# Kernel tuning notes

Measured on AMD Instinct MI355X. Metric: run time of the kernel, lower is better.

## Reference

```python
import jax, jax.numpy as jnp
import numpy as np

N, E, EL = 20000, 320000, 100000
IN, HID, OUT, H = 256, 128, 128, 4
NEG_SLOPE = 0.2


def setup_inputs() -> dict:
    key = jax.random.key(0)
    ks = jax.random.split(key, 20)
    g = lambda k, shape, fan: jax.random.normal(k, shape, jnp.float32) * (1.0 / np.sqrt(fan))
    inp = {
        'x': jax.random.normal(ks[0], (N, IN), jnp.float32),
        'edge_index': jax.random.randint(ks[1], (2, E), 0, N, jnp.int32),
        'edge_label_index': jax.random.randint(ks[2], (2, EL), 0, N, jnp.int32),
        # GATv2 layer 1: in -> hidden, heads=H, concat
        'W_l1': g(ks[3], (IN, H * HID), IN), 'b_l1': jnp.zeros((H * HID,), jnp.float32),
        'W_r1': g(ks[4], (IN, H * HID), IN), 'b_r1': jnp.zeros((H * HID,), jnp.float32),
        'att1': g(ks[5], (H, HID), HID), 'bias1': jnp.zeros((H * HID,), jnp.float32),
        # GATv2 layer 2: H*hidden -> out, heads=1
        'W_l2': g(ks[6], (H * HID, OUT), H * HID), 'b_l2': jnp.zeros((OUT,), jnp.float32),
        'W_r2': g(ks[7], (H * HID, OUT), H * HID), 'b_r2': jnp.zeros((OUT,), jnp.float32),
        'att2': g(ks[8], (1, OUT), OUT), 'bias2': jnp.zeros((OUT,), jnp.float32),
        # decoder: Linear(2*OUT, HID) -> GELU -> Linear(HID, 1)
        'W_d1': g(ks[9], (2 * OUT, HID), 2 * OUT), 'b_d1': jnp.zeros((HID,), jnp.float32),
        'W_d2': g(ks[10], (HID, 1), HID), 'b_d2': jnp.zeros((1,), jnp.float32),
    }
    return inp


def gatv2_conv(x, src, dst, Wl, bl, Wr, br, att, bias, heads, ch):
    n = x.shape[0]
    xl = (x @ Wl + bl).reshape(n, heads, ch)  # source transform
    xr = (x @ Wr + br).reshape(n, heads, ch)  # target transform
    xj = xl[src]                              # [E, H, C] messages from source
    xi = xr[dst]                              # [E, H, C]
    e = jax.nn.leaky_relu(xi + xj, NEG_SLOPE)
    logits = jnp.einsum('ehc,hc->eh', e, att)  # [E, H]
    # segment softmax over incoming edges of each target node
    m = jax.ops.segment_max(logits, dst, num_segments=n)
    a = jnp.exp(logits - m[dst])
    s = jax.ops.segment_sum(a, dst, num_segments=n)
    alpha = a / s[dst]
    out = jax.ops.segment_sum(alpha[..., None] * xj, dst, num_segments=n)
    return out.reshape(n, heads * ch) + bias


def reference(x, edge_index, edge_label_index,
              W_l1, b_l1, W_r1, b_r1, att1, bias1,
              W_l2, b_l2, W_r2, b_r2, att2, bias2,
              W_d1, b_d1, W_d2, b_d2):
    n = x.shape[0]
    loops = jnp.arange(n, dtype=edge_index.dtype)
    src = jnp.concatenate([edge_index[0], loops])  # add_self_loops=True (PyG default)
    dst = jnp.concatenate([edge_index[1], loops])
    z = gatv2_conv(x, src, dst, W_l1, b_l1, W_r1, b_r1, att1, bias1, H, HID)
    z = jax.nn.gelu(z)  # dropout is identity in eval mode
    z = gatv2_conv(z, src, dst, W_l2, b_l2, W_r2, b_r2, att2, bias2, 1, OUT)
    # link decoder: gather-concat-MLP
    h = jnp.concatenate([z[edge_label_index[0]], z[edge_label_index[1]]], axis=-1)
    h = jax.nn.gelu(h @ W_d1 + b_d1)
    return (h @ W_d2 + b_d2).squeeze(-1)
```

## Files before the change

kernel.cpp:

```cpp
#include <hip/hip_runtime.h>
#include <hip/hip_bf16.h>
#include <math.h>
#include <stdint.h>

using bf16 = __hip_bfloat16;
typedef unsigned short u16;
typedef unsigned int   u32;
typedef __attribute__((ext_vector_type(8))) short short8;
typedef __attribute__((ext_vector_type(4))) float f32x4;
typedef _Float16 h2 __attribute__((ext_vector_type(2)));

static constexpr int NN   = 20000;
static constexpr int EE   = 320000;
static constexpr int ELN  = 100000;
static constexpr int ETOT = EE + NN;
static constexpr int INC  = 256;
static constexpr int C1   = 512;
static constexpr int C2   = 128;
static constexpr int NB   = (NN + 255) / 256;

__device__ __forceinline__ float us2f(u16 u){ union{u32 i; float f;}x; x.i=((u32)u)<<16; return x.f; }
__device__ __forceinline__ u16  f2us(float f){ union{bf16 h; u16 u;}c; c.h=__float2bfloat16(f); return c.u; }
__device__ __forceinline__ float h2f(u16 u){ union{u16 u; _Float16 h;}c; c.u=u; return (float)c.h; }
__device__ __forceinline__ float gelu_f(float x){
  float u = 1.5957691216057308f*(x + 0.044715f*x*x*x);
  float ex = __expf(u);
  float th = 1.f - 2.f/(ex + 1.f);
  return 0.5f*x*(1.f+th);
}
__device__ __forceinline__ void gl_lds16(const u16* g, void* l) {
  __builtin_amdgcn_global_load_lds((const __attribute__((address_space(1))) void*)g,
                                   (__attribute__((address_space(3))) void*)l, 16, 0, 0);
}
__device__ __forceinline__ void ld4v(const float* p, float* o){ float4 v=*(const float4*)p; o[0]=v.x;o[1]=v.y;o[2]=v.z;o[3]=v.w; }
__device__ __forceinline__ void ld4v(const u16* p, float* o){ uint2 v=*(const uint2*)p;
  o[0]=us2f(v.x&0xffff);o[1]=us2f(v.x>>16);o[2]=us2f(v.y&0xffff);o[3]=us2f(v.y>>16); }
__device__ __forceinline__ void ld4v(const _Float16* p, float* o){ uint2 v=*(const uint2*)p;
  o[0]=h2f(v.x&0xffff);o[1]=h2f(v.x>>16);o[2]=h2f(v.y&0xffff);o[3]=h2f(v.y>>16); }
__device__ __forceinline__ void ld8v(const float* p, float* o){ ld4v(p,o); ld4v(p+4,o+4); }
__device__ __forceinline__ void ld8v(const u16* p, float* o){ uint4 v=*(const uint4*)p;
  o[0]=us2f(v.x&0xffff);o[1]=us2f(v.x>>16);o[2]=us2f(v.y&0xffff);o[3]=us2f(v.y>>16);
  o[4]=us2f(v.z&0xffff);o[5]=us2f(v.z>>16);o[6]=us2f(v.w&0xffff);o[7]=us2f(v.w>>16); }
__device__ __forceinline__ void ld8v(const _Float16* p, float* o){ uint4 v=*(const uint4*)p;
  o[0]=h2f(v.x&0xffff);o[1]=h2f(v.x>>16);o[2]=h2f(v.y&0xffff);o[3]=h2f(v.y>>16);
  o[4]=h2f(v.z&0xffff);o[5]=h2f(v.z>>16);o[6]=h2f(v.w&0xffff);o[7]=h2f(v.w>>16); }
__device__ __forceinline__ void ld2v(const float* p, float* o){ float2 v=*(const float2*)p; o[0]=v.x;o[1]=v.y; }
__device__ __forceinline__ void ld2v(const _Float16* p, float* o){ u32 w=*(const u32*)p;
  o[0]=h2f(w&0xffff); o[1]=h2f(w>>16); }
__device__ __forceinline__ void st4v(float* p, const float* v){ *(float4*)p = make_float4(v[0],v[1],v[2],v[3]); }
__device__ __forceinline__ void st4v(u16* p, const float* v){ uint2 o;
  o.x=f2us(v[0])|((u32)f2us(v[1])<<16); o.y=f2us(v[2])|((u32)f2us(v[3])<<16); *(uint2*)p=o; }
__device__ __forceinline__ void st8v(float* p, const float* v){ st4v(p,v); st4v(p+4,v+4); }
__device__ __forceinline__ void st8v(u16* p, const float* v){ uint4 o;
  o.x=f2us(v[0])|((u32)f2us(v[1])<<16); o.y=f2us(v[2])|((u32)f2us(v[3])<<16);
  o.z=f2us(v[4])|((u32)f2us(v[5])<<16); o.w=f2us(v[6])|((u32)f2us(v[7])<<16); *(uint4*)p=o; }

struct PrepArgs {
  const float* x; u16* xth; u16* xtl; int nx;
  const float* wsrc[5]; u16* wth[5]; u16* wtl[5]; int wK[5]; int wN[5];
  const int* ei; int* cnt;
};
__global__ __launch_bounds__(256) void k_prep(PrepArgs a) {
  int seg = blockIdx.y;
  int tid = blockIdx.x*256 + threadIdx.x;
  int stride = gridDim.x*256;
  if (seg == 0) {
    for (int i = tid; i < a.nx; i += stride) {
      float v = a.x[i];
      u16 h = f2us(v);
      a.xth[i] = h;
      a.xtl[i] = f2us(v - us2f(h));
    }
  } else if (seg <= 5) {
    int s = seg - 1;
    int K = a.wK[s], N = a.wN[s];
    int n = K * N;
    for (int i = tid; i < n; i += stride) {
      int nn = i / K, k = i - nn*K;
      float v = a.wsrc[s][(size_t)k*N + nn];
      u16 h = f2us(v);
      a.wth[s][i] = h;
      a.wtl[s][i] = f2us(v - us2f(h));
    }
  } else {
    for (int e = tid; e < ETOT; e += stride) {
      int d = (e < EE) ? a.ei[EE + e] : (e - EE);
      if ((u32)d < (u32)NN) atomicAdd(&a.cnt[d], 1);
    }
  }
}

__global__ void k_scan_a(const int* __restrict__ cnt, int* __restrict__ row_ptr,
                         int* __restrict__ bsum) {
  __shared__ int buf[256];
  int idx = blockIdx.x*256 + threadIdx.x;
  int v = (idx < NN) ? cnt[idx] : 0;
  buf[threadIdx.x] = v;
  __syncthreads();
  for (int off = 1; off < 256; off <<= 1) {
    int t = (threadIdx.x >= off) ? buf[threadIdx.x - off] : 0;
    __syncthreads();
    buf[threadIdx.x] += t;
    __syncthreads();
  }
  if (idx < NN) row_ptr[idx] = buf[threadIdx.x] - v;
  if (threadIdx.x == 255) bsum[blockIdx.x] = buf[255];
}
__global__ void k_scan_b(int* __restrict__ bsum, int* __restrict__ row_ptr) {
  __shared__ int buf[128];
  int v = (threadIdx.x < NB) ? bsum[threadIdx.x] : 0;
  buf[threadIdx.x] = v;
  __syncthreads();
  for (int off = 1; off < 128; off <<= 1) {
    int t = (threadIdx.x >= off) ? buf[threadIdx.x - off] : 0;
    __syncthreads();
    buf[threadIdx.x] += t;
    __syncthreads();
  }
  if (threadIdx.x < NB) bsum[threadIdx.x] = buf[threadIdx.x] - v;
  if (threadIdx.x == 127) row_ptr[NN] = buf[127];
}
__global__ void k_scan_c(int* __restrict__ row_ptr, const int* __restrict__ bsum,
                         int* __restrict__ cur) {
  int idx = blockIdx.x*256 + threadIdx.x;
  if (idx < NN) {
    int v = row_ptr[idx] + bsum[blockIdx.x];
    row_ptr[idx] = v;
    cur[idx] = v;
  }
}
__global__ void k_scatter(const int* __restrict__ ei, int* __restrict__ cur,
                          int* __restrict__ col) {
  int e = blockIdx.x*blockDim.x + threadIdx.x;
  if (e < ETOT) {
    int s, d;
    if (e < EE) { s = ei[e]; d = ei[EE + e]; } else { s = d = e - EE; }
    if ((u32)d >= (u32)NN) d = 0;
    int pos = atomicAdd(&cur[d], 1);
    if ((u32)pos < (u32)ETOT) col[pos] = s;
  }
}

__global__ __launch_bounds__(256, 3)
void k_mgemm_a(const u16* __restrict__ Ath, const u16* __restrict__ Atl,
               const u16* __restrict__ Bth, const u16* __restrict__ Btl,
               const float* __restrict__ biasA, const float* __restrict__ biasB, int ncut,
               _Float16* __restrict__ C, int M, int N, int K, int nby) {
  __shared__ __align__(16) u16 sm[17408];
  int tid = threadIdx.x;
  int bidy = blockIdx.x % nby, bidx = blockIdx.x / nby;
  int m0 = bidx * 128, n0 = bidy * 128;
  int wave = tid >> 6, lane = tid & 63;
  int wm = (wave & 1) * 64, wn = (wave >> 1) * 64;
  int l15 = lane & 15, quad = lane >> 4;
  const u16* pbase = (wave == 0) ? Ath : (wave == 1) ? Atl : (wave == 2) ? Bth : Btl;
  bool isA = wave < 2;
  int rbase = isA ? m0 : n0;
  int rseg = lane >> 2;
  int kseg = (lane & 3) * 8;
  f32x4 acc[4][4] = {};
  for (int k0 = 0; k0 < K; k0 += 32) {
    #pragma unroll
    for (int i = 0; i < 8; ++i) {
      int r = rbase + i*16 + rseg;
      if (isA && r > M-1) r = M-1;
      gl_lds16(&pbase[(size_t)r*K + k0 + kseg], (char*)sm + (wave<<13) + (i<<10));
    }
    __syncthreads();
    short8 af_h[4], af_l[4], bf_h[4], bf_l[4];
    #pragma unroll
    for (int i = 0; i < 4; ++i) {
      af_h[i] = *(const short8*)&sm[         (wm + i*16 + l15)*32 + quad*8];
      af_l[i] = *(const short8*)&sm[ 4096 +  (wm + i*16 + l15)*32 + quad*8];
      bf_h[i] = *(const short8*)&sm[ 8192 +  (wn + i*16 + l15)*32 + quad*8];
      bf_l[i] = *(const short8*)&sm[12288 +  (wn + i*16 + l15)*32 + quad*8];
    }
    #pragma unroll
    for (int i = 0; i < 4; ++i)
      #pragma unroll
      for (int j = 0; j < 4; ++j) {
        acc[i][j] = __builtin_amdgcn_mfma_f32_16x16x32_bf16(af_h[i], bf_l[j], acc[i][j], 0,0,0);
        acc[i][j] = __builtin_amdgcn_mfma_f32_16x16x32_bf16(af_l[i], bf_h[j], acc[i][j], 0,0,0);
        acc[i][j] = __builtin_amdgcn_mfma_f32_16x16x32_bf16(af_h[i], bf_h[j], acc[i][j], 0,0,0);
      }
    __syncthreads();
  }
  #pragma unroll
  for (int j = 0; j < 4; ++j) {
    int col = wn + j*16 + l15;
    int colg = n0 + col;
    float bv = (colg < ncut) ? biasA[colg] : biasB[colg - ncut];
    #pragma unroll
    for (int i = 0; i < 4; ++i) {
      int rowb = wm + i*16 + quad*4;
      #pragma unroll
      for (int r = 0; r < 4; ++r) {
        union { _Float16 h; u16 u; } cv;
        cv.h = (_Float16)(acc[i][j][r] + bv);
        sm[(rowb + r)*136 + col] = cv.u;
      }
    }
  }
  __syncthreads();
  int row = tid >> 1, half = (tid & 1) * 64;
  int gr = m0 + row;
  if (gr < M) {
    uint4* d = (uint4*)&C[(size_t)gr*N + n0 + half];
    const uint4* s = (const uint4*)&sm[row*136 + half];
    #pragma unroll
    for (int q = 0; q < 8; ++q) d[q] = s[q];
  }
}

__global__ __launch_bounds__(256, 3)
void k_dec3(const _Float16* __restrict__ z2,
            const int* __restrict__ eli,
            const u16* __restrict__ Wth, const u16* __restrict__ Wtl,
            const float* __restrict__ bd1,
            const float* __restrict__ Wd2, const float* __restrict__ bd2,
            float* __restrict__ out) {
  __shared__ __align__(16) u16 Ah[128][32], Al[128][32];
  __shared__ __align__(16) u16 Bh[128][32], Bl[128][32];
  __shared__ float pr[128][2];
  int tid = threadIdx.x;
  int e0 = blockIdx.x * 128;
  int wave = tid >> 6, lane = tid & 63;
  int wm = (wave & 1) * 64, wn = (wave >> 1) * 64;
  int l15 = lane & 15, quad = lane >> 4;
  int ar = tid >> 3;
  int ak = (tid & 7) * 4;
  int bn = tid >> 2;
  int bc = (tid & 3) * 8;
  int ia4[4], ib4[4];
  #pragma unroll
  for (int i = 0; i < 4; ++i) {
    int e = e0 + ar + 32*i;
    bool ev = e < ELN;
    int a = ev ? eli[e] : 0;      if ((u32)a >= (u32)NN) a = 0;
    int b = ev ? eli[ELN+e] : 0;  if ((u32)b >= (u32)NN) b = 0;
    ia4[i] = a; ib4[i] = b;
  }
  f32x4 acc[4][4] = {};
  for (int k0 = 0; k0 < 256; k0 += 32) {
    #pragma unroll
    for (int i = 0; i < 4; ++i) {
      int row = ar + 32*i;
      int kk = k0 + ak;
      const _Float16* src = (kk < 128) ? &z2[(size_t)ia4[i]*128 + kk]
                                       : &z2[(size_t)ib4[i]*128 + (kk - 128)];
      float hv[4];
      ld4v(src, hv);
      u16 hi[4], lo[4];
      #pragma unroll
      for (int j = 0; j < 4; ++j) {
        hi[j] = f2us(hv[j]);
        lo[j] = f2us(hv[j] - us2f(hi[j]));
      }
      *(uint2*)&Ah[row][ak] = make_uint2(hi[0]|((u32)hi[1]<<16), hi[2]|((u32)hi[3]<<16));
      *(uint2*)&Al[row][ak] = make_uint2(lo[0]|((u32)lo[1]<<16), lo[2]|((u32)lo[3]<<16));
    }
    #pragma unroll
    for (int i = 0; i < 2; ++i) {
      int n = bn + 64*i;
      *(uint4*)&Bh[n][bc] = *(const uint4*)&Wth[(size_t)n*256 + k0 + bc];
      *(uint4*)&Bl[n][bc] = *(const uint4*)&Wtl[(size_t)n*256 + k0 + bc];
    }
    __syncthreads();
    short8 af_h[4], af_l[4], bf_h[4], bf_l[4];
    #pragma unroll
    for (int i = 0; i < 4; ++i) {
      af_h[i] = *(const short8*)&Ah[wm + i*16 + l15][quad*8];
      af_l[i] = *(const short8*)&Al[wm + i*16 + l15][quad*8];
      bf_h[i] = *(const short8*)&Bh[wn + i*16 + l15][quad*8];
      bf_l[i] = *(const short8*)&Bl[wn + i*16 + l15][quad*8];
    }
    #pragma unroll
    for (int i = 0; i < 4; ++i)
      #pragma unroll
      for (int j = 0; j < 4; ++j) {
        acc[i][j] = __builtin_amdgcn_mfma_f32_16x16x32_bf16(af_h[i], bf_l[j], acc[i][j], 0,0,0);
        acc[i][j] = __builtin_amdgcn_mfma_f32_16x16x32_bf16(af_l[i], bf_h[j], acc[i][j], 0,0,0);
        acc[i][j] = __builtin_amdgcn_mfma_f32_16x16x32_bf16(af_h[i], bf_h[j], acc[i][j], 0,0,0);
      }
    __syncthreads();
  }
  float w2c[4], bbc[4];
  #pragma unroll
  for (int j = 0; j < 4; ++j) {
    int col = wn + j*16 + l15;
    w2c[j] = Wd2[col];
    bbc[j] = bd1[col];
  }
  #pragma unroll
  for (int i = 0; i < 4; ++i) {
    #pragma unroll
    for (int r = 0; r < 4; ++r) {
      float part = 0.f;
      #pragma unroll
      for (int j = 0; j < 4; ++j)
        part += gelu_f(acc[i][j][r] + bbc[j]) * w2c[j];
      part += __shfl_xor(part,1); part += __shfl_xor(part,2);
      part += __shfl_xor(part,4); part += __shfl_xor(part,8);
      if (l15 == 0) pr[wm + i*16 + quad*4 + r][wn>>6] = part;
    }
  }
  __syncthreads();
  if (tid < 128) {
    int e = e0 + tid;
    if (e < ELN) out[e] = pr[tid][0] + pr[tid][1] + bd2[0];
  }
}

__global__ __launch_bounds__(256) void k_edge1p(const _Float16* __restrict__ xl,
                                                const _Float16* __restrict__ xr, int ld,
                                                const float* __restrict__ att,
                                                const float* __restrict__ bias,
                                                const int* __restrict__ row_ptr,
                                                const int* __restrict__ col,
                                                u16* __restrict__ z1h, u16* __restrict__ z1l) {
  int wid = (blockIdx.x*blockDim.x + threadIdx.x) >> 6;
  if (wid >= NN) return;
  int lane = threadIdx.x & 63;
  int c8 = lane*8;
  union Q { uint4 u; h2 h[4]; };
  Q XI; XI.u = *(const uint4*)&xr[(size_t)wid*ld + c8];
  h2 at[4];
  #pragma unroll
  for (int k=0;k<4;++k) { at[k][0] = (_Float16)att[c8+2*k]; at[k][1] = (_Float16)att[c8+2*k+1]; }
  const h2 k02 = {(_Float16)0.2f, (_Float16)0.2f};
  float acc[8] = {};
  float s = 0.f;
  int e0 = __builtin_amdgcn_readfirstlane(row_ptr[wid]);
  int e1 = __builtin_amdgcn_readfirstlane(row_ptr[wid+1]);
  int e = e0;
  for (; e + 4 <= e1; e += 4) {
    int s1 = __builtin_amdgcn_readfirstlane(col[e]);   if ((u32)s1 >= (u32)NN) s1 = 0;
    int s2 = __builtin_amdgcn_readfirstlane(col[e+1]); if ((u32)s2 >= (u32)NN) s2 = 0;
    int s3 = __builtin_amdgcn_readfirstlane(col[e+2]); if ((u32)s3 >= (u32)NN) s3 = 0;
    int s4 = __builtin_amdgcn_readfirstlane(col[e+3]); if ((u32)s4 >= (u32)NN) s4 = 0;
    Q X1, X2, X3, X4;
    X1.u = *(const uint4*)&xl[(size_t)s1*ld + c8];
    X2.u = *(const uint4*)&xl[(size_t)s2*ld + c8];
    X3.u = *(const uint4*)&xl[(size_t)s3*ld + c8];
    X4.u = *(const uint4*)&xl[(size_t)s4*ld + c8];
    float p1 = 0.f, p2 = 0.f, p3 = 0.f, p4 = 0.f;
    #pragma unroll
    for (int k=0;k<4;++k) {
      h2 t1 = XI.h[k] + X1.h[k]; t1 = __builtin_elementwise_max(t1, t1*k02);
      p1 = __builtin_amdgcn_fdot2(t1, at[k], p1, false);
      h2 t2 = XI.h[k] + X2.h[k]; t2 = __builtin_elementwise_max(t2, t2*k02);
      p2 = __builtin_amdgcn_fdot2(t2, at[k], p2, false);
      h2 t3 = XI.h[k] + X3.h[k]; t3 = __builtin_elementwise_max(t3, t3*k02);
      p3 = __builtin_amdgcn_fdot2(t3, at[k], p3, false);
      h2 t4 = XI.h[k] + X4.h[k]; t4 = __builtin_elementwise_max(t4, t4*k02);
      p4 = __builtin_amdgcn_fdot2(t4, at[k], p4, false);
    }
    p1 += __shfl_xor(p1,1); p2 += __shfl_xor(p2,1); p3 += __shfl_xor(p3,1); p4 += __shfl_xor(p4,1);
    p1 += __shfl_xor(p1,2); p2 += __shfl_xor(p2,2); p3 += __shfl_xor(p3,2); p4 += __shfl_xor(p4,2);
    p1 += __shfl_xor(p1,4); p2 += __shfl_xor(p2,4); p3 += __shfl_xor(p3,4); p4 += __shfl_xor(p4,4);
    p1 += __shfl_xor(p1,8); p2 += __shfl_xor(p2,8); p3 += __shfl_xor(p3,8); p4 += __shfl_xor(p4,8);
    float w1 = __expf(p1), w2 = __expf(p2), w3 = __expf(p3), w4 = __expf(p4);
    s += (w1 + w2) + (w3 + w4);
    #pragma unroll
    for (int k=0;k<4;++k) {
      acc[2*k]   += (w1*(float)X1.h[k][0] + w2*(float)X2.h[k][0])
                  + (w3*(float)X3.h[k][0] + w4*(float)X4.h[k][0]);
      acc[2*k+1] += (w1*(float)X1.h[k][1] + w2*(float)X2.h[k][1])
                  + (w3*(float)X3.h[k][1] + w4*(float)X4.h[k][1]);
    }
  }
  for (; e < e1; ++e) {
    int sn = __builtin_amdgcn_readfirstlane(col[e]); if ((u32)sn >= (u32)NN) sn = 0;
    Q XJ; XJ.u = *(const uint4*)&xl[(size_t)sn*ld + c8];
    float p = 0.f;
    #pragma unroll
    for (int k=0;k<4;++k) {
      h2 t = XI.h[k] + XJ.h[k];
      t = __builtin_elementwise_max(t, t*k02);
      p = __builtin_amdgcn_fdot2(t, at[k], p, false);
    }
    p += __shfl_xor(p,1); p += __shfl_xor(p,2);
    p += __shfl_xor(p,4); p += __shfl_xor(p,8);
    float w = __expf(p);
    s += w;
    #pragma unroll
    for (int k=0;k<4;++k) {
      acc[2*k]   += w*(float)XJ.h[k][0];
      acc[2*k+1] += w*(float)XJ.h[k][1];
    }
  }
  float inv = 1.f/s;
  u16 hh[8], ll[8];
  #pragma unroll
  for (int j=0;j<8;++j) {
    float o = gelu_f(acc[j]*inv + bias[c8+j]);
    hh[j] = f2us(o);
    ll[j] = f2us(o - us2f(hh[j]));
  }
  uint4 H, L;
  H.x = hh[0]|((u32)hh[1]<<16); H.y = hh[2]|((u32)hh[3]<<16);
  H.z = hh[4]|((u32)hh[5]<<16); H.w = hh[6]|((u32)hh[7]<<16);
  L.x = ll[0]|((u32)ll[1]<<16); L.y = ll[2]|((u32)ll[3]<<16);
  L.z = ll[4]|((u32)ll[5]<<16); L.w = ll[6]|((u32)ll[7]<<16);
  *(uint4*)&z1h[(size_t)wid*C1 + c8] = H;
  *(uint4*)&z1l[(size_t)wid*C1 + c8] = L;
}

__global__ __launch_bounds__(256) void k_edge2p(const _Float16* __restrict__ xl,
                                                const _Float16* __restrict__ xr, int ld,
                                                const float* __restrict__ att,
                                                const float* __restrict__ bias,
                                                const int* __restrict__ row_ptr,
                                                const int* __restrict__ col,
                                                _Float16* __restrict__ z2) {
  int wid = (blockIdx.x*blockDim.x + threadIdx.x) >> 6;
  if (wid >= NN) return;
  int lane = threadIdx.x & 63;
  int c2 = lane*2;
  union W { u32 u; h2 h; };
  W XI; XI.u = *(const u32*)&xr[(size_t)wid*ld + c2];
  h2 at; at[0] = (_Float16)att[c2]; at[1] = (_Float16)att[c2+1];
  const h2 k02 = {(_Float16)0.2f, (_Float16)0.2f};
  float s = 0.f, ac0 = 0.f, ac1 = 0.f;
  int e0 = __builtin_amdgcn_readfirstlane(row_ptr[wid]);
  int e1 = __builtin_amdgcn_readfirstlane(row_ptr[wid+1]);
  int e = e0;
  for (; e + 4 <= e1; e += 4) {
    int s1 = __builtin_amdgcn_readfirstlane(col[e]);   if ((u32)s1 >= (u32)NN) s1 = 0;
    int s2 = __builtin_amdgcn_readfirstlane(col[e+1]); if ((u32)s2 >= (u32)NN) s2 = 0;
    int s3 = __builtin_amdgcn_readfirstlane(col[e+2]); if ((u32)s3 >= (u32)NN) s3 = 0;
    int s4 = __builtin_amdgcn_readfirstlane(col[e+3]); if ((u32)s4 >= (u32)NN) s4 = 0;
    W X1, X2, X3, X4;
    X1.u = *(const u32*)&xl[(size_t)s1*ld + c2];
    X2.u = *(const u32*)&xl[(size_t)s2*ld + c2];
    X3.u = *(const u32*)&xl[(size_t)s3*ld + c2];
    X4.u = *(const u32*)&xl[(size_t)s4*ld + c2];
    h2 t1 = XI.h + X1.h; t1 = __builtin_elementwise_max(t1, t1*k02);
    h2 t2 = XI.h + X2.h; t2 = __builtin_elementwise_max(t2, t2*k02);
    h2 t3 = XI.h + X3.h; t3 = __builtin_elementwise_max(t3, t3*k02);
    h2 t4 = XI.h + X4.h; t4 = __builtin_elementwise_max(t4, t4*k02);
    float p1 = __builtin_amdgcn_fdot2(t1, at, 0.f, false);
    float p2 = __builtin_amdgcn_fdot2(t2, at, 0.f, false);
    float p3 = __builtin_amdgcn_fdot2(t3, at, 0.f, false);
    float p4 = __builtin_amdgcn_fdot2(t4, at, 0.f, false);
    p1 += __shfl_xor(p1,1);  p2 += __shfl_xor(p2,1);  p3 += __shfl_xor(p3,1);  p4 += __shfl_xor(p4,1);
    p1 += __shfl_xor(p1,2);  p2 += __shfl_xor(p2,2);  p3 += __shfl_xor(p3,2);  p4 += __shfl_xor(p4,2);
    p1 += __shfl_xor(p1,4);  p2 += __shfl_xor(p2,4);  p3 += __shfl_xor(p3,4);  p4 += __shfl_xor(p4,4);
    p1 += __shfl_xor(p1,8);  p2 += __shfl_xor(p2,8);  p3 += __shfl_xor(p3,8);  p4 += __shfl_xor(p4,8);
    p1 += __shfl_xor(p1,16); p2 += __shfl_xor(p2,16); p3 += __shfl_xor(p3,16); p4 += __shfl_xor(p4,16);
    p1 += __shfl_xor(p1,32); p2 += __shfl_xor(p2,32); p3 += __shfl_xor(p3,32); p4 += __shfl_xor(p4,32);
    float w1 = __expf(p1), w2 = __expf(p2), w3 = __expf(p3), w4 = __expf(p4);
    s += (w1 + w2) + (w3 + w4);
    ac0 += (w1*(float)X1.h[0] + w2*(float)X2.h[0]) + (w3*(float)X3.h[0] + w4*(float)X4.h[0]);
    ac1 += (w1*(float)X1.h[1] + w2*(float)X2.h[1]) + (w3*(float)X3.h[1] + w4*(float)X4.h[1]);
  }
  for (; e < e1; ++e) {
    int sn = __builtin_amdgcn_readfirstlane(col[e]); if ((u32)sn >= (u32)NN) sn = 0;
    W XJ; XJ.u = *(const u32*)&xl[(size_t)sn*ld + c2];
    h2 t = XI.h + XJ.h;
    t = __builtin_elementwise_max(t, t*k02);
    float p = __builtin_amdgcn_fdot2(t, at, 0.f, false);
    p += __shfl_xor(p,1);  p += __shfl_xor(p,2);
    p += __shfl_xor(p,4);  p += __shfl_xor(p,8);
    p += __shfl_xor(p,16); p += __shfl_xor(p,32);
    float w = __expf(p);
    s += w;
    ac0 += w*(float)XJ.h[0];
    ac1 += w*(float)XJ.h[1];
  }
  float inv = 1.f/s;
  union { h2 h; u32 u; } o;
  o.h[0] = (_Float16)(ac0*inv + bias[c2]);
  o.h[1] = (_Float16)(ac1*inv + bias[c2+1]);
  *(u32*)&z2[(size_t)wid*C2 + c2] = o.u;
}

__global__ void k_hist(const int* __restrict__ ei, int* __restrict__ cnt) {
  int e = blockIdx.x*blockDim.x + threadIdx.x;
  if (e < ETOT) {
    int d = (e < EE) ? ei[EE + e] : (e - EE);
    if ((u32)d < (u32)NN) atomicAdd(&cnt[d], 1);
  }
}
template <typename AT, typename CT>
__global__ __launch_bounds__(256) void k_gemm(const AT* __restrict__ A,
                                              const float* __restrict__ W,
                                              const float* __restrict__ bias,
                                              CT* __restrict__ C,
                                              int M, int Nc, int K) {
  __shared__ __align__(16) float As[16][64];
  __shared__ __align__(16) float Bs[16][64];
  int tid = threadIdx.x;
  int m0 = blockIdx.x*64, n0 = blockIdx.y*64;
  int ty = tid >> 4, tx = tid & 15;
  int lrow = tid >> 2;
  int lk   = (tid & 3)*4;
  int wk   = tid >> 4;
  int wn   = (tid & 15)*4;
  float acc[4][4] = {};
  for (int k0 = 0; k0 < K; k0 += 16) {
    int row = m0 + lrow;
    if (row < M) {
      float a4[4]; ld4v(&A[(size_t)row*K + k0 + lk], a4);
      As[lk+0][lrow]=a4[0]; As[lk+1][lrow]=a4[1]; As[lk+2][lrow]=a4[2]; As[lk+3][lrow]=a4[3];
    } else {
      #pragma unroll
      for (int j=0;j<4;++j) As[lk+j][lrow]=0.f;
    }
    {
      float4 bv4 = *(const float4*)&W[(size_t)(k0+wk)*Nc + n0 + wn];
      Bs[wk][wn+0]=bv4.x; Bs[wk][wn+1]=bv4.y; Bs[wk][wn+2]=bv4.z; Bs[wk][wn+3]=bv4.w;
    }
    __syncthreads();
    #pragma unroll
    for (int kk=0;kk<16;++kk) {
      float4 av = *(const float4*)&As[kk][ty*4];
      float4 bv = *(const float4*)&Bs[kk][tx*4];
      float a[4]={av.x,av.y,av.z,av.w}, b[4]={bv.x,bv.y,bv.z,bv.w};
      #pragma unroll
      for (int i=0;i<4;++i)
        #pragma unroll
        for (int j=0;j<4;++j)
          acc[i][j] += a[i]*b[j];
    }
    __syncthreads();
  }
  float bv[4];
  #pragma unroll
  for (int j=0;j<4;++j) bv[j] = bias[n0 + tx*4 + j];
  #pragma unroll
  for (int i=0;i<4;++i) {
    int row = m0 + ty*4 + i;
    if (row < M) {
      float o4[4] = {acc[i][0]+bv[0], acc[i][1]+bv[1], acc[i][2]+bv[2], acc[i][3]+bv[3]};
      st4v(&C[(size_t)row*Nc + n0 + tx*4], o4);
    }
  }
}
template <typename TI, typename TO>
__global__ __launch_bounds__(256) void k_edge1c(const TI* __restrict__ xl,
                                                const TI* __restrict__ xr, int ld,
                                                const float* __restrict__ att,
                                                const float* __restrict__ bias,
                                                const int* __restrict__ row_ptr,
                                                const int* __restrict__ col,
                                                TO* __restrict__ z1) {
  int wid = (blockIdx.x*blockDim.x + threadIdx.x) >> 6;
  if (wid >= NN) return;
  int lane = threadIdx.x & 63;
  int c8 = lane*8;
  float xi[8], av[8], acc[8] = {};
  ld8v(&xr[(size_t)wid*ld + c8], xi);
  #pragma unroll
  for (int j=0;j<8;++j) av[j] = att[c8+j];
  float s = 0.f;
  int e0 = row_ptr[wid], e1 = row_ptr[wid+1];
  for (int e = e0; e < e1; ++e) {
    int sn = col[e]; if ((u32)sn >= (u32)NN) sn = 0;
    float xj[8];
    ld8v(&xl[(size_t)sn*ld + c8], xj);
    float p = 0.f;
    #pragma unroll
    for (int j=0;j<8;++j) {
      float t = xi[j] + xj[j];
      t = fmaxf(t, 0.2f*t);
      p += t*av[j];
    }
    p += __shfl_xor(p,1); p += __shfl_xor(p,2);
    p += __shfl_xor(p,4); p += __shfl_xor(p,8);
    float w = __expf(p);
    s += w;
    #pragma unroll
    for (int j=0;j<8;++j) acc[j] += w*xj[j];
  }
  float inv = 1.f/s, o[8];
  #pragma unroll
  for (int j=0;j<8;++j) o[j] = gelu_f(acc[j]*inv + bias[c8+j]);
  st8v(&z1[(size_t)wid*C1 + c8], o);
}
template <typename TI, typename TO>
__global__ __launch_bounds__(256) void k_edge2c(const TI* __restrict__ xl,
                                                const TI* __restrict__ xr, int ld,
                                                const float* __restrict__ att,
                                                const float* __restrict__ bias,
                                                const int* __restrict__ row_ptr,
                                                const int* __restrict__ col,
                                                TO* __restrict__ z2) {
  int wid = (blockIdx.x*blockDim.x + threadIdx.x) >> 6;
  if (wid >= NN) return;
  int lane = threadIdx.x & 63;
  int c2 = lane*2;
  float xiv[2];
  ld2v(&xr[(size_t)wid*ld + c2], xiv);
  float a0 = att[c2], a1 = att[c2+1];
  float s = 0.f, ac0 = 0.f, ac1 = 0.f;
  int e0 = row_ptr[wid], e1 = row_ptr[wid+1];
  for (int e = e0; e < e1; ++e) {
    int sn = col[e]; if ((u32)sn >= (u32)NN) sn = 0;
    float xj[2];
    ld2v(&xl[(size_t)sn*ld + c2], xj);
    float t0 = xiv[0] + xj[0]; t0 = fmaxf(t0, 0.2f*t0);
    float t1 = xiv[1] + xj[1]; t1 = fmaxf(t1, 0.2f*t1);
    float p = t0*a0 + t1*a1;
    p += __shfl_xor(p,1);  p += __shfl_xor(p,2);
    p += __shfl_xor(p,4);  p += __shfl_xor(p,8);
    p += __shfl_xor(p,16); p += __shfl_xor(p,32);
    float w = __expf(p);
    s += w;
    ac0 += w*xj[0];
    ac1 += w*xj[1];
  }
  float inv = 1.f/s;
  z2[(size_t)wid*C2 + c2]   = (TO)(ac0*inv + bias[c2]);
  z2[(size_t)wid*C2 + c2+1] = (TO)(ac1*inv + bias[c2+1]);
}
__global__ __launch_bounds__(256) void k_dec2(const float* __restrict__ z2,
                                              const int* __restrict__ eli,
                                              const float* __restrict__ Wd1,
                                              const float* __restrict__ bd1,
                                              const float* __restrict__ Wd2,
                                              const float* __restrict__ bd2,
                                              float* __restrict__ out) {
  __shared__ __align__(16) float As[16][64];
  __shared__ __align__(16) float Bs[16][128];
  int tid = threadIdx.x;
  int e0 = blockIdx.x * 64;
  int ty = tid >> 4, tx = tid & 15;
  int lrow = tid >> 2;
  int lk   = (tid & 3) * 4;
  int wk   = tid >> 4;
  int wn   = (tid & 15) * 8;
  int e = e0 + lrow;
  bool ev = e < ELN;
  int ia = ev ? eli[e] : 0;       if ((u32)ia >= (u32)NN) ia = 0;
  int ib = ev ? eli[ELN+e] : 0;   if ((u32)ib >= (u32)NN) ib = 0;
  float acc[4][8] = {};
  for (int k0 = 0; k0 < 256; k0 += 16) {
    int kk4 = k0 + lk;
    const float* src = (kk4 < 128) ? &z2[(size_t)ia*128 + kk4]
                                   : &z2[(size_t)ib*128 + (kk4 - 128)];
    float4 a4 = ev ? *(const float4*)src : make_float4(0.f,0.f,0.f,0.f);
    As[lk+0][lrow]=a4.x; As[lk+1][lrow]=a4.y; As[lk+2][lrow]=a4.z; As[lk+3][lrow]=a4.w;
    *(float4*)&Bs[wk][wn]   = *(const float4*)&Wd1[(size_t)(k0+wk)*128 + wn];
    *(float4*)&Bs[wk][wn+4] = *(const float4*)&Wd1[(size_t)(k0+wk)*128 + wn + 4];
    __syncthreads();
    #pragma unroll
    for (int kk = 0; kk < 16; ++kk) {
      float4 av = *(const float4*)&As[kk][ty*4];
      float a[4] = {av.x, av.y, av.z, av.w};
      float4 b0 = *(const float4*)&Bs[kk][tx*4];
      float4 b1 = *(const float4*)&Bs[kk][64 + tx*4];
      float b[8] = {b0.x,b0.y,b0.z,b0.w,b1.x,b1.y,b1.z,b1.w};
      #pragma unroll
      for (int i = 0; i < 4; ++i)
        #pragma unroll
        for (int j = 0; j < 8; ++j)
          acc[i][j] += a[i]*b[j];
    }
    __syncthreads();
  }
  float w2[8], bb[8];
  #pragma unroll
  for (int j = 0; j < 4; ++j) {
    w2[j]   = Wd2[tx*4+j];      bb[j]   = bd1[tx*4+j];
    w2[j+4] = Wd2[64+tx*4+j];   bb[j+4] = bd1[64+tx*4+j];
  }
  float b2 = bd2[0];
  #pragma unroll
  for (int i = 0; i < 4; ++i) {
    float part = 0.f;
    #pragma unroll
    for (int j = 0; j < 8; ++j)
      part += gelu_f(acc[i][j] + bb[j]) * w2[j];
    part += __shfl_xor(part,1); part += __shfl_xor(part,2);
    part += __shfl_xor(part,4); part += __shfl_xor(part,8);
    int row = e0 + ty*4 + i;
    if (tx == 0 && row < ELN) out[row] = part + b2;
  }
}

__global__ void k_tiny(float* out, float code) {
  if (threadIdx.x == 0) out[0] = code;
}

extern "C" void kernel_launch(void* const* d_in, const int* in_sizes, int n_in,
                              void* d_out, int out_size, void* d_ws, size_t ws_size,
                              hipStream_t stream) {
  const float* x     = (const float*)d_in[0];
  const int*   ei    = (const int*)  d_in[1];
  const int*   eli   = (const int*)  d_in[2];
  const float* Wl1   = (const float*)d_in[3];
  const float* bl1   = (const float*)d_in[4];
  const float* Wr1   = (const float*)d_in[5];
  const float* br1   = (const float*)d_in[6];
  const float* att1  = (const float*)d_in[7];
  const float* bias1 = (const float*)d_in[8];
  const float* Wl2   = (const float*)d_in[9];
  const float* bl2   = (const float*)d_in[10];
  const float* Wr2   = (const float*)d_in[11];
  const float* br2   = (const float*)d_in[12];
  const float* att2  = (const float*)d_in[13];
  const float* bias2 = (const float*)d_in[14];
  const float* Wd1   = (const float*)d_in[15];
  const float* bd1   = (const float*)d_in[16];
  const float* Wd2   = (const float*)d_in[17];
  const float* bd2   = (const float*)d_in[18];
  float* out = (float*)d_out;

  constexpr size_t INTW = (size_t)(NN+1) + NN + ETOT;
  constexpr size_t FULL_WORDS = 3ull*NN*C1 + INTW;
  constexpr size_t CMP_WORDS  = 3ull*NN*C1/2 + INTW;

  bool full    = ws_size >= FULL_WORDS*4;
  bool compact = !full && ws_size >= CMP_WORDS*4;
  if (!full && !compact) {
    size_t mb = ws_size >> 20;
    k_tiny<<<1, 64, 0, stream>>>(out, 16384.f + (float)mb);
    return;
  }

  size_t regA = full ? (size_t)NN*C1 : (size_t)NN*C1/2;
  char* base = (char*)d_ws;
  void* wA = base;
  void* wB = base + regA*4;
  void* wC = base + 2*regA*4;
  int* row_ptr = (int*)(base + 3*regA*4);
  int* cnt     = row_ptr + (NN + 1);
  int* col     = cnt + NN;
  int* bsum    = (int*)wA;

  hipMemsetAsync(cnt, 0, NN*sizeof(int), stream);

  if (full) {
    _Float16* xlr1 = (_Float16*)wA;
    _Float16* xlr2 = (_Float16*)wA;
    u16* xth = (u16*)wB;
    u16* xtl = xth + (size_t)NN*INC;
    u16* wt1th = (u16*)((char*)wB + (21u<<20));
    u16* wt1tl = wt1th + 1024*256;
    u16* wt2th = wt1tl + 1024*256;
    u16* wt2tl = wt2th + 256*512;
    u16* wdth  = wt2tl + 256*512;
    u16* wdtl  = wdth  + 128*256;
    u16* z1h = (u16*)wC;
    u16* z1l = z1h + (size_t)NN*C1;
    _Float16* z2 = (_Float16*)wC;

    PrepArgs pa;
    pa.x = x; pa.xth = xth; pa.xtl = xtl; pa.nx = NN*INC;
    pa.wsrc[0]=Wl1; pa.wth[0]=wt1th;         pa.wtl[0]=wt1tl;         pa.wK[0]=INC; pa.wN[0]=C1;
    pa.wsrc[1]=Wr1; pa.wth[1]=wt1th+512*256; pa.wtl[1]=wt1tl+512*256; pa.wK[1]=INC; pa.wN[1]=C1;
    pa.wsrc[2]=Wl2; pa.wth[2]=wt2th;         pa.wtl[2]=wt2tl;         pa.wK[2]=C1;  pa.wN[2]=C2;
    pa.wsrc[3]=Wr2; pa.wth[3]=wt2th+128*512; pa.wtl[3]=wt2tl+128*512; pa.wK[3]=C1;  pa.wN[3]=C2;
    pa.wsrc[4]=Wd1; pa.wth[4]=wdth;          pa.wtl[4]=wdtl;          pa.wK[4]=256; pa.wN[4]=C2;
    pa.ei = ei; pa.cnt = cnt;
    k_prep<<<dim3(1344, 7), 256, 0, stream>>>(pa);

    k_scan_a<<<NB, 256, 0, stream>>>(cnt, row_ptr, bsum);
    k_scan_b<<<1, 128, 0, stream>>>(bsum, row_ptr);
    k_scan_c<<<NB, 256, 0, stream>>>(row_ptr, bsum, cnt);
    k_scatter<<<(ETOT+255)/256, 256, 0, stream>>>(ei, cnt, col);

    k_mgemm_a<<<157*8, 256, 0, stream>>>(xth, xtl, wt1th, wt1tl,
                                         bl1, br1, 512, xlr1, NN, 1024, INC, 8);
    k_edge1p<<<NN/4, 256, 0, stream>>>(xlr1, xlr1+512, 1024, att1, bias1, row_ptr, col, z1h, z1l);
    k_mgemm_a<<<157*2, 256, 0, stream>>>(z1h, z1l, wt2th, wt2tl,
                                         bl2, br2, 128, xlr2, NN, 256, C1, 2);
    k_edge2p<<<NN/4, 256, 0, stream>>>(xlr2, xlr2+128, 256, att2, bias2, row_ptr, col, z2);
    k_dec3<<<(ELN+127)/128, 256, 0, stream>>>(z2, eli, wdth, wdtl, bd1, Wd2, bd2, out);
  } else {
    u16* xl1 = (u16*)wA;
    u16* xr1 = (u16*)wB;
    u16* z1  = (u16*)wC;
    float* xl2 = (float*)wA;
    float* xr2 = (float*)wB;
    float* z2  = (float*)wC;
    k_hist<<<(ETOT+255)/256, 256, 0, stream>>>(ei, cnt);
    k_scan_a<<<NB, 256, 0, stream>>>(cnt, row_ptr, bsum);
    k_scan_b<<<1, 128, 0, stream>>>(bsum, row_ptr);
    k_scan_c<<<NB, 256, 0, stream>>>(row_ptr, bsum, cnt);
    k_scatter<<<(ETOT+255)/256, 256, 0, stream>>>(ei, cnt, col);
    dim3 g1((NN+63)/64, C1/64);
    dim3 g2((NN+63)/64, C2/64);
    k_gemm<float,u16><<<g1, 256, 0, stream>>>(x, Wl1, bl1, xl1, NN, C1, INC);
    k_gemm<float,u16><<<g1, 256, 0, stream>>>(x, Wr1, br1, xr1, NN, C1, INC);
    k_edge1c<u16,u16><<<NN/4, 256, 0, stream>>>(xl1, xr1, C1, att1, bias1, row_ptr, col, z1);
    k_gemm<u16,float><<<g2, 256, 0, stream>>>(z1, Wl2, bl2, xl2, NN, C2, C1);
    k_gemm<u16,float><<<g2, 256, 0, stream>>>(z1, Wr2, br2, xr2, NN, C2, C1);
    k_edge2c<float,float><<<NN/4, 256, 0, stream>>>(xl2, xr2, C2, att2, bias2, row_ptr, col, z2);
    k_dec2<<<(ELN+63)/64, 256, 0, stream>>>(z2, eli, Wd1, bd1, Wd2, bd2, out);
  }
}
```

Measured before the change: 344.7 us.

## Split decoder linear into per-node projections before gathering edge pairs

```diff
diff --git a/kernel.cpp b/kernel.cpp
--- a/kernel.cpp
+++ b/kernel.cpp
@@ -57,7 +57,7 @@
 
 struct PrepArgs {
   const float* x; u16* xth; u16* xtl; int nx;
-  const float* wsrc[5]; u16* wth[5]; u16* wtl[5]; int wK[5]; int wN[5];
+  const float* wsrc[6]; u16* wth[6]; u16* wtl[6]; int wK[6]; int wN[6];
   const int* ei; int* cnt;
 };
 __global__ __launch_bounds__(256) void k_prep(PrepArgs a) {
@@ -71,7 +71,7 @@
       a.xth[i] = h;
       a.xtl[i] = f2us(v - us2f(h));
     }
-  } else if (seg <= 5) {
+  } else if (seg <= 6) {
     int s = seg - 1;
     int K = a.wK[s], N = a.wN[s];
     int n = K * N;
@@ -189,7 +189,7 @@
   for (int j = 0; j < 4; ++j) {
     int col = wn + j*16 + l15;
     int colg = n0 + col;
-    float bv = (colg < ncut) ? biasA[colg] : biasB[colg - ncut];
+    float bv = (colg < ncut) ? biasA[colg] : (biasB ? biasB[colg - ncut] : 0.f);
     #pragma unroll
     for (int i = 0; i < 4; ++i) {
       int rowb = wm + i*16 + quad*4;
@@ -212,102 +212,28 @@
   }
 }
 
-__global__ __launch_bounds__(256, 3)
-void k_dec3(const _Float16* __restrict__ z2,
-            const int* __restrict__ eli,
-            const u16* __restrict__ Wth, const u16* __restrict__ Wtl,
-            const float* __restrict__ bd1,
-            const float* __restrict__ Wd2, const float* __restrict__ bd2,
-            float* __restrict__ out) {
-  __shared__ __align__(16) u16 Ah[128][32], Al[128][32];
-  __shared__ __align__(16) u16 Bh[128][32], Bl[128][32];
-  __shared__ float pr[128][2];
-  int tid = threadIdx.x;
-  int e0 = blockIdx.x * 128;
-  int wave = tid >> 6, lane = tid & 63;
-  int wm = (wave & 1) * 64, wn = (wave >> 1) * 64;
-  int l15 = lane & 15, quad = lane >> 4;
-  int ar = tid >> 3;
-  int ak = (tid & 7) * 4;
-  int bn = tid >> 2;
-  int bc = (tid & 3) * 8;
-  int ia4[4], ib4[4];
-  #pragma unroll
-  for (int i = 0; i < 4; ++i) {
-    int e = e0 + ar + 32*i;
-    bool ev = e < ELN;
-    int a = ev ? eli[e] : 0;      if ((u32)a >= (u32)NN) a = 0;
-    int b = ev ? eli[ELN+e] : 0;  if ((u32)b >= (u32)NN) b = 0;
-    ia4[i] = a; ib4[i] = b;
-  }
-  f32x4 acc[4][4] = {};
-  for (int k0 = 0; k0 < 256; k0 += 32) {
-    #pragma unroll
-    for (int i = 0; i < 4; ++i) {
-      int row = ar + 32*i;
-      int kk = k0 + ak;
-      const _Float16* src = (kk < 128) ? &z2[(size_t)ia4[i]*128 + kk]
-                                       : &z2[(size_t)ib4[i]*128 + (kk - 128)];
-      float hv[4];
-      ld4v(src, hv);
-      u16 hi[4], lo[4];
-      #pragma unroll
-      for (int j = 0; j < 4; ++j) {
-        hi[j] = f2us(hv[j]);
-        lo[j] = f2us(hv[j] - us2f(hi[j]));
-      }
-      *(uint2*)&Ah[row][ak] = make_uint2(hi[0]|((u32)hi[1]<<16), hi[2]|((u32)hi[3]<<16));
-      *(uint2*)&Al[row][ak] = make_uint2(lo[0]|((u32)lo[1]<<16), lo[2]|((u32)lo[3]<<16));
-    }
-    #pragma unroll
-    for (int i = 0; i < 2; ++i) {
-      int n = bn + 64*i;
-      *(uint4*)&Bh[n][bc] = *(const uint4*)&Wth[(size_t)n*256 + k0 + bc];
-      *(uint4*)&Bl[n][bc] = *(const uint4*)&Wtl[(size_t)n*256 + k0 + bc];
-    }
-    __syncthreads();
-    short8 af_h[4], af_l[4], bf_h[4], bf_l[4];
-    #pragma unroll
-    for (int i = 0; i < 4; ++i) {
-      af_h[i] = *(const short8*)&Ah[wm + i*16 + l15][quad*8];
-      af_l[i] = *(const short8*)&Al[wm + i*16 + l15][quad*8];
-      bf_h[i] = *(const short8*)&Bh[wn + i*16 + l15][quad*8];
-      bf_l[i] = *(const short8*)&Bl[wn + i*16 + l15][quad*8];
-    }
-    #pragma unroll
-    for (int i = 0; i < 4; ++i)
-      #pragma unroll
-      for (int j = 0; j < 4; ++j) {
-        acc[i][j] = __builtin_amdgcn_mfma_f32_16x16x32_bf16(af_h[i], bf_l[j], acc[i][j], 0,0,0);
-        acc[i][j] = __builtin_amdgcn_mfma_f32_16x16x32_bf16(af_l[i], bf_h[j], acc[i][j], 0,0,0);
-        acc[i][j] = __builtin_amdgcn_mfma_f32_16x16x32_bf16(af_h[i], bf_h[j], acc[i][j], 0,0,0);
-      }
-    __syncthreads();
-  }
-  float w2c[4], bbc[4];
-  #pragma unroll
-  for (int j = 0; j < 4; ++j) {
-    int col = wn + j*16 + l15;
-    w2c[j] = Wd2[col];
-    bbc[j] = bd1[col];
-  }
-  #pragma unroll
-  for (int i = 0; i < 4; ++i) {
-    #pragma unroll
-    for (int r = 0; r < 4; ++r) {
-      float part = 0.f;
-      #pragma unroll
-      for (int j = 0; j < 4; ++j)
-        part += gelu_f(acc[i][j][r] + bbc[j]) * w2c[j];
-      part += __shfl_xor(part,1); part += __shfl_xor(part,2);
-      part += __shfl_xor(part,4); part += __shfl_xor(part,8);
-      if (l15 == 0) pr[wm + i*16 + quad*4 + r][wn>>6] = part;
-    }
-  }
-  __syncthreads();
-  if (tid < 128) {
-    int e = e0 + tid;
-    if (e < ELN) out[e] = pr[tid][0] + pr[tid][1] + bd2[0];
+__global__ __launch_bounds__(256) void k_dec5(const _Float16* __restrict__ UV,
+                                              const int* __restrict__ eli,
+                                              const float* __restrict__ Wd2,
+                                              const float* __restrict__ bd2,
+                                              float* __restrict__ out) {
+  int gw = (blockIdx.x*256 + threadIdx.x) >> 6;
+  int nw = (gridDim.x*256) >> 6;
+  int lane = threadIdx.x & 63;
+  int c2 = lane*2;
+  float w2a = Wd2[c2], w2b = Wd2[c2+1];
+  float b2 = bd2[0];
+  for (int e = gw; e < ELN; e += nw) {
+    int a = __builtin_amdgcn_readfirstlane(eli[e]);      if ((u32)a >= (u32)NN) a = 0;
+    int b = __builtin_amdgcn_readfirstlane(eli[ELN+e]);  if ((u32)b >= (u32)NN) b = 0;
+    float u[2], v[2];
+    ld2v(&UV[(size_t)a*256 + c2], u);
+    ld2v(&UV[(size_t)b*256 + 128 + c2], v);
+    float p = gelu_f(u[0]+v[0])*w2a + gelu_f(u[1]+v[1])*w2b;
+    p += __shfl_xor(p,1);  p += __shfl_xor(p,2);
+    p += __shfl_xor(p,4);  p += __shfl_xor(p,8);
+    p += __shfl_xor(p,16); p += __shfl_xor(p,32);
+    if (lane == 0) out[e] = p + b2;
   }
 }
 
@@ -412,7 +338,7 @@
                                                 const float* __restrict__ bias,
                                                 const int* __restrict__ row_ptr,
                                                 const int* __restrict__ col,
-                                                _Float16* __restrict__ z2) {
+                                                u16* __restrict__ z2h, u16* __restrict__ z2l) {
   int wid = (blockIdx.x*blockDim.x + threadIdx.x) >> 6;
   if (wid >= NN) return;
   int lane = threadIdx.x & 63;
@@ -469,10 +395,12 @@
     ac1 += w*(float)XJ.h[1];
   }
   float inv = 1.f/s;
-  union { h2 h; u32 u; } o;
-  o.h[0] = (_Float16)(ac0*inv + bias[c2]);
-  o.h[1] = (_Float16)(ac1*inv + bias[c2+1]);
-  *(u32*)&z2[(size_t)wid*C2 + c2] = o.u;
+  float o0 = ac0*inv + bias[c2];
+  float o1 = ac1*inv + bias[c2+1];
+  u16 h0 = f2us(o0), h1 = f2us(o1);
+  u16 l0 = f2us(o0 - us2f(h0)), l1v = f2us(o1 - us2f(h1));
+  *(u32*)&z2h[(size_t)wid*C2 + c2] = h0 | ((u32)h1 << 16);
+  *(u32*)&z2l[(size_t)wid*C2 + c2] = l0 | ((u32)l1v << 16);
 }
 
 __global__ void k_hist(const int* __restrict__ ei, int* __restrict__ cnt) {
@@ -734,6 +662,7 @@
   if (full) {
     _Float16* xlr1 = (_Float16*)wA;
     _Float16* xlr2 = (_Float16*)wA;
+    _Float16* UV   = (_Float16*)wA;
     u16* xth = (u16*)wB;
     u16* xtl = xth + (size_t)NN*INC;
     u16* wt1th = (u16*)((char*)wB + (21u<<20));
@@ -741,20 +670,22 @@
     u16* wt2th = wt1tl + 1024*256;
     u16* wt2tl = wt2th + 256*512;
     u16* wdth  = wt2tl + 256*512;
-    u16* wdtl  = wdth  + 128*256;
+    u16* wdtl  = wdth  + 256*128;
     u16* z1h = (u16*)wC;
     u16* z1l = z1h + (size_t)NN*C1;
-    _Float16* z2 = (_Float16*)wC;
+    u16* z2h = (u16*)wC;
+    u16* z2l = z2h + (size_t)NN*C2;
 
     PrepArgs pa;
     pa.x = x; pa.xth = xth; pa.xtl = xtl; pa.nx = NN*INC;
-    pa.wsrc[0]=Wl1; pa.wth[0]=wt1th;         pa.wtl[0]=wt1tl;         pa.wK[0]=INC; pa.wN[0]=C1;
-    pa.wsrc[1]=Wr1; pa.wth[1]=wt1th+512*256; pa.wtl[1]=wt1tl+512*256; pa.wK[1]=INC; pa.wN[1]=C1;
-    pa.wsrc[2]=Wl2; pa.wth[2]=wt2th;         pa.wtl[2]=wt2tl;         pa.wK[2]=C1;  pa.wN[2]=C2;
-    pa.wsrc[3]=Wr2; pa.wth[3]=wt2th+128*512; pa.wtl[3]=wt2tl+128*512; pa.wK[3]=C1;  pa.wN[3]=C2;
-    pa.wsrc[4]=Wd1; pa.wth[4]=wdth;          pa.wtl[4]=wdtl;          pa.wK[4]=256; pa.wN[4]=C2;
+    pa.wsrc[0]=Wl1;          pa.wth[0]=wt1th;         pa.wtl[0]=wt1tl;         pa.wK[0]=INC; pa.wN[0]=C1;
+    pa.wsrc[1]=Wr1;          pa.wth[1]=wt1th+512*256; pa.wtl[1]=wt1tl+512*256; pa.wK[1]=INC; pa.wN[1]=C1;
+    pa.wsrc[2]=Wl2;          pa.wth[2]=wt2th;         pa.wtl[2]=wt2tl;         pa.wK[2]=C1;  pa.wN[2]=C2;
+    pa.wsrc[3]=Wr2;          pa.wth[3]=wt2th+128*512; pa.wtl[3]=wt2tl+128*512; pa.wK[3]=C1;  pa.wN[3]=C2;
+    pa.wsrc[4]=Wd1;          pa.wth[4]=wdth;          pa.wtl[4]=wdtl;          pa.wK[4]=128; pa.wN[4]=128;
+    pa.wsrc[5]=Wd1+128*128;  pa.wth[5]=wdth+128*128;  pa.wtl[5]=wdtl+128*128;  pa.wK[5]=128; pa.wN[5]=128;
     pa.ei = ei; pa.cnt = cnt;
-    k_prep<<<dim3(1344, 7), 256, 0, stream>>>(pa);
+    k_prep<<<dim3(1344, 8), 256, 0, stream>>>(pa);
 
     k_scan_a<<<NB, 256, 0, stream>>>(cnt, row_ptr, bsum);
     k_scan_b<<<1, 128, 0, stream>>>(bsum, row_ptr);
@@ -766,8 +697,10 @@
     k_edge1p<<<NN/4, 256, 0, stream>>>(xlr1, xlr1+512, 1024, att1, bias1, row_ptr, col, z1h, z1l);
     k_mgemm_a<<<157*2, 256, 0, stream>>>(z1h, z1l, wt2th, wt2tl,
                                          bl2, br2, 128, xlr2, NN, 256, C1, 2);
-    k_edge2p<<<NN/4, 256, 0, stream>>>(xlr2, xlr2+128, 256, att2, bias2, row_ptr, col, z2);
-    k_dec3<<<(ELN+127)/128, 256, 0, stream>>>(z2, eli, wdth, wdtl, bd1, Wd2, bd2, out);
+    k_edge2p<<<NN/4, 256, 0, stream>>>(xlr2, xlr2+128, 256, att2, bias2, row_ptr, col, z2h, z2l);
+    k_mgemm_a<<<157*2, 256, 0, stream>>>(z2h, z2l, wdth, wdtl,
+                                         bd1, nullptr, 128, UV, NN, 256, 128, 2);
+    k_dec5<<<2048, 256, 0, stream>>>(UV, eli, Wd2, bd2, out);
   } else {
     u16* xl1 = (u16*)wA;
     u16* xr1 = (u16*)wB;
```

Measured after the change: 347.8 us. No clear change (+0.9%).
